# Kernel tuning notes

Measured on AMD Instinct MI355X. Metric: run time of the kernel, lower is better.

The kernel has to match this reference:

```python
import jax, jax.numpy as jnp
import numpy as np

C = 64          # channels (init arg)
G = 64          # input latent grid side -> output grid side 2G = 128
S = 2 * G + 2   # padded side for injective key encoding (coords shifted by +1)
N_IN = 60_000


def _encode(coords):
    # injective int32 key for 3D coords in [-1, 2G]
    c = coords + 1
    return (c[:, 0] * S + c[:, 1]) * S + c[:, 2]


def _lookup(keys_sorted, order, query_keys):
    # returns (row index into original arrays, found mask)
    n = keys_sorted.shape[0]
    pos = jnp.clip(jnp.searchsorted(keys_sorted, query_keys), 0, n - 1)
    found = keys_sorted[pos] == query_keys
    return order[pos], found


def _sparse_conv(out_coords, feats, W, b, keys_sorted, order, offsets):
    # Minkowski stride-1 conv: out[i] = sum_k feats[nbr(i, off_k)] @ W[k] + b
    acc = jnp.zeros((out_coords.shape[0], W.shape[-1]), feats.dtype)
    for k in range(offsets.shape[0]):  # 27 fixed kernel offsets
        idx, found = _lookup(keys_sorted, order, _encode(out_coords + offsets[k]))
        nb = jnp.where(found[:, None], feats[idx], jnp.zeros((), feats.dtype))
        acc = acc + nb @ W[k]
    return acc + b


def setup_inputs() -> dict:
    rng = np.random.default_rng(0)
    lin = rng.choice(G ** 3, size=N_IN, replace=False)  # unique occupied voxels
    coords = np.stack([lin // (G * G), (lin // G) % G, lin % G], axis=1).astype(np.int32)
    key = jax.random.key(0)
    ks = jax.random.split(key, 7)
    sc = 0.05
    return {
        'coords': jnp.asarray(coords),
        'feats': jax.random.normal(ks[0], (N_IN, C), jnp.float32),
        'W_up': jax.random.normal(ks[1], (8, C, C), jnp.float32) * sc,
        'b_up': jax.random.normal(ks[2], (C,), jnp.float32) * sc,
        'W1': jax.random.normal(ks[3], (27, C, C), jnp.float32) * sc,
        'b1': jax.random.normal(ks[4], (C,), jnp.float32) * sc,
        'W2': jax.random.normal(ks[5], (27, C, C), jnp.float32) * sc,
        'b2': jax.random.normal(ks[6], (C,), jnp.float32) * sc,
    }


def reference(coords, feats, W_up, b_up, W1, b1, W2, b2):
    # generative transpose conv (kernel 2, stride 2): 8 unique children per voxel
    child = jnp.array([[i, j, k] for i in (0, 1) for j in (0, 1) for k in (0, 1)], jnp.int32)
    out_coords = (2 * coords[:, None, :] + child[None]).reshape(-1, 3)  # [8N, 3]
    x = jnp.einsum('nc,kcd->nkd', feats, W_up).reshape(-1, C) + b_up     # [8N, C]
    x = jax.nn.relu(x)
    # shared kernel-map structure for both stride-1 convs
    keys = _encode(out_coords)
    order = jnp.argsort(keys)
    keys_sorted = keys[order]
    offs = jnp.array([[i, j, k] for i in (-1, 0, 1) for j in (-1, 0, 1) for k in (-1, 0, 1)], jnp.int32)
    x = jax.nn.relu(_sparse_conv(out_coords, x, W1, b1, keys_sorted, order, offs))
    x = _sparse_conv(out_coords, x, W2, b2, keys_sorted, order, offs)
    return x
```

## Files before the change

### kernel.cpp

```cpp
#include <hip/hip_runtime.h>
#include <stdint.h>

typedef __bf16 bf16x8 __attribute__((ext_vector_type(8)));
typedef float f32x4 __attribute__((ext_vector_type(4)));
typedef unsigned short ushort_t;

#define NPARENT 60000
#define NOUT (NPARENT*8)
#define ZIDX NOUT
#define TBL_N (66*66*66)
#define NBIN 4096

static constexpr size_t OFF_TABLE = 0;
static constexpr size_t OFF_CS    = 1152000;
static constexpr size_t OFF_Y     = OFF_CS + 960000;
static constexpr size_t OFF_HIST  = OFF_Y;
static constexpr size_t OFF_CNT   = OFF_Y + 16384;
static constexpr size_t OFF_Z     = OFF_Y + (size_t)(NOUT+1)*128;
static constexpr size_t OFF_FEATB = OFF_Z + (size_t)(NOUT+1)*128;
static constexpr size_t OFF_WUPF  = OFF_FEATB + (size_t)NPARENT*128;
static constexpr size_t OFF_W1F   = OFF_WUPF + (size_t)8*8192;
static constexpr size_t OFF_W2F   = OFF_W1F + (size_t)27*8192;
static constexpr size_t WS_NEED   = OFF_W2F + (size_t)27*8192;

__device__ __forceinline__ ushort_t f2bf(float x) {
  uint32_t u = __float_as_uint(x);
  u += 0x7fffu + ((u >> 16) & 1u);
  return (ushort_t)(u >> 16);
}

__device__ __forceinline__ int binof(int x, int y, int z) {
  int bx = x >> 2, by = y >> 2, bz = z >> 2, m = 0;
  #pragma unroll
  for (int b = 0; b < 4; ++b)
    m |= (((bx>>b)&1) << (3*b+2)) | (((by>>b)&1) << (3*b+1)) | (((bz>>b)&1) << (3*b));
  return m;
}

__device__ __forceinline__ void gl2lds16(const void* g, void* l) {
  __builtin_amdgcn_global_load_lds(
      (const __attribute__((address_space(1))) uint32_t*)g,
      (__attribute__((address_space(3))) uint32_t*)l, 16, 0, 0);
}

__global__ void k_zero(ushort_t* y, ushort_t* z) {
  int t = threadIdx.x;
  if (t < 64) y[(size_t)ZIDX*64 + t] = 0;
  else        z[(size_t)ZIDX*64 + (t-64)] = 0;
}

__global__ void k_hist(const int* __restrict__ coords, int* __restrict__ hist) {
  int i = blockIdx.x*blockDim.x + threadIdx.x;
  if (i >= NPARENT) return;
  atomicAdd(&hist[binof(coords[3*i], coords[3*i+1], coords[3*i+2])], 1);
}

__global__ void k_scan(const int* __restrict__ hist, int* __restrict__ cnt) {
  __shared__ int s[256];
  int t = threadIdx.x;
  int loc[16], sum = 0;
  #pragma unroll
  for (int j=0;j<16;++j){ loc[j]=hist[t*16+j]; sum+=loc[j]; }
  s[t]=sum;
  __syncthreads();
  if (t==0){ int a=0; for (int i=0;i<256;++i){ int v=s[i]; s[i]=a; a+=v; } }
  __syncthreads();
  int a=s[t];
  #pragma unroll
  for (int j=0;j<16;++j){ cnt[t*16+j]=a; a+=loc[j]; }
}

__global__ void k_rank(const int* __restrict__ coords, int* __restrict__ cnt,
                       int4* __restrict__ cs, int* __restrict__ tbl) {
  int i = blockIdx.x*blockDim.x + threadIdx.x;
  if (i >= NPARENT) return;
  int x = coords[3*i], y = coords[3*i+1], z = coords[3*i+2];
  int r = atomicAdd(&cnt[binof(x,y,z)], 1);
  cs[r] = make_int4(x, y, z, i);
  tbl[((x+1)*66 + (y+1))*66 + (z+1)] = r;
}

__global__ void k_feats_bf16(const float4* __restrict__ f, const int4* __restrict__ cs,
                             ushort_t* __restrict__ o, int total) {
  int t = blockIdx.x*blockDim.x + threadIdx.x;
  if (t >= total) return;
  int p = t >> 4, q = t & 15;
  int i = cs[p].w;
  float4 v = f[(size_t)i*16 + q];
  size_t ob = (size_t)p*64 + q*4;
  o[ob+0] = f2bf(v.x); o[ob+1] = f2bf(v.y);
  o[ob+2] = f2bf(v.z); o[ob+3] = f2bf(v.w);
}

__global__ void k_wfrag(const float* __restrict__ w, ushort_t* __restrict__ o, int total) {
  int i = blockIdx.x*blockDim.x + threadIdx.x;
  if (i >= total) return;
  int k = i >> 12, r = i & 4095, c = r >> 6, d = r & 63;
  int nt = d >> 4, lp = d & 15, ks = c >> 5, hi = (c >> 3) & 3, e = c & 7;
  int fi = ks*4 + nt, lane = hi*16 + lp;
  o[(size_t)(k*8 + fi)*512 + lane*8 + e] = f2bf(w[i]);
}

__global__ __launch_bounds__(256) void k_up(const ushort_t* __restrict__ featb,
    const ushort_t* __restrict__ wupf, const float* __restrict__ bup,
    ushort_t* __restrict__ y)
{
  int wave = threadIdx.x >> 6, lane = threadIdx.x & 63;
  int n0 = blockIdx.x*64 + wave*16;
  if (n0 >= NPARENT) return;
  int lp = lane & 15, hi = lane >> 4;
  const ushort_t* ar = featb + (size_t)(n0+lp)*64 + hi*8;
  bf16x8 a0 = *(const bf16x8*)(ar);
  bf16x8 a1 = *(const bf16x8*)(ar + 32);
  float bv[4];
  #pragma unroll
  for (int nt=0; nt<4; ++nt) bv[nt] = bup[nt*16+lp];
  for (int c8=0; c8<8; ++c8) {
    const ushort_t* wb = wupf + (size_t)c8*4096 + lane*8;
    f32x4 acc[4];
    #pragma unroll
    for (int nt=0;nt<4;++nt) acc[nt] = (f32x4){0.f,0.f,0.f,0.f};
    #pragma unroll
    for (int nt=0;nt<4;++nt)
      acc[nt] = __builtin_amdgcn_mfma_f32_16x16x32_bf16(a0, *(const bf16x8*)(wb + nt*512), acc[nt], 0,0,0);
    #pragma unroll
    for (int nt=0;nt<4;++nt)
      acc[nt] = __builtin_amdgcn_mfma_f32_16x16x32_bf16(a1, *(const bf16x8*)(wb + (4+nt)*512), acc[nt], 0,0,0);
    #pragma unroll
    for (int nt=0;nt<4;++nt) {
      #pragma unroll
      for (int j=0;j<4;++j) {
        int par = n0 + hi*4 + j;
        float v = acc[nt][j] + bv[nt];
        v = fmaxf(v, 0.f);
        y[(size_t)(par*8 + c8)*64 + nt*16 + lp] = f2bf(v);
      }
    }
  }
}

template<int RELU, int SCATTER, typename OUT_T>
__global__ __launch_bounds__(256) void k_conv(const int4* __restrict__ cs,
    const int* __restrict__ tbl, const ushort_t* __restrict__ fin,
    const ushort_t* __restrict__ wf, const float* __restrict__ bias,
    OUT_T* __restrict__ out)
{
  __shared__ __align__(16) int nbrs[32*27];
  __shared__ __align__(16) ushort_t bbuf[2][4096];

  int bid = blockIdx.x;
  int xcd = bid & 7, jj = bid >> 3;
  int wg = (xcd < 3 ? xcd*235 : 705 + (xcd-3)*234) + jj;

  int tid = threadIdx.x;
  int wave = tid >> 6, lane = tid & 63;
  int m0 = wg*256 + wave*64;
  int lp = lane & 15, hi = lane >> 4;
  int pblk0 = wg*32;

  for (int i = tid; i < 32*27; i += 256) {
    int p = i / 27, j = i - p*27;
    int4 cc = cs[pblk0 + p];
    int dx = j/9 - 1, dy = (j/3)%3 - 1, dz = j%3 - 1;
    nbrs[i] = tbl[((cc.x+dx+1)*66 + (cc.y+dy+1))*66 + (cc.z+dz+1)];
  }

  {
    const char* wb = (const char*)wf;
    #pragma unroll
    for (int j=0;j<2;++j) {
      int chunk = wave*2 + j;
      gl2lds16(wb + (size_t)chunk*1024 + lane*16, &bbuf[0][chunk*512]);
    }
  }

  int cx = (lp>>2)&1, cy = (lp>>1)&1, cz = lp&1, c = lp&7;
  int plbase = wave*8 + (lp>>3);

  f32x4 acc[4][4];
  #pragma unroll
  for (int s=0;s<4;++s)
    #pragma unroll
    for (int nt=0;nt<4;++nt) acc[s][nt] = (f32x4){0.f,0.f,0.f,0.f};

  const char* finl = (const char*)fin + hi*16;

  __syncthreads();

  uint32_t aoffc[4];
  {
    int idx = ((cx-1)>>1)*9 + ((cy-1)>>1)*3 + ((cz-1)>>1) + 13;
    int cpx = c ^ 7;
    #pragma unroll
    for (int s=0;s<4;++s) {
      int rank = nbrs[(plbase + s*2)*27 + idx];
      uint32_t off = (uint32_t)(rank*8 + cpx) * 128u;
      aoffc[s] = (rank < 0) ? (uint32_t)ZIDX*128u : off;
    }
  }

  #pragma unroll 1
  for (int k=0;k<27;++k) {
    int cur = k & 1;
    bf16x8 a[4][2];
    #pragma unroll
    for (int s=0;s<4;++s) {
      a[s][0] = *(const bf16x8*)(finl + aoffc[s]);
      a[s][1] = *(const bf16x8*)(finl + aoffc[s] + 64);
    }
    if (k < 26) {
      const char* wb = (const char*)wf + (size_t)(k+1)*8192;
      #pragma unroll
      for (int j=0;j<2;++j) {
        int chunk = wave*2 + j;
        gl2lds16(wb + (size_t)chunk*1024 + lane*16, &bbuf[cur^1][chunk*512]);
      }
    }
    bf16x8 bfr[8];
    #pragma unroll
    for (int f=0;f<8;++f) bfr[f] = *(const bf16x8*)&bbuf[cur][f*512 + lane*8];
    uint32_t aoffn[4];
    if (k < 26) {
      int k2 = k+1;
      int ox = k2/9 - 1, oy = (k2/3)%3 - 1, oz = k2%3 - 1;
      int xk = ((ox&1)<<2) | ((oy&1)<<1) | (oz&1);
      int cpx = c ^ xk;
      int idx = ((cx+ox)>>1)*9 + ((cy+oy)>>1)*3 + ((cz+oz)>>1) + 13;
      #pragma unroll
      for (int s=0;s<4;++s) {
        int rank = nbrs[(plbase + s*2)*27 + idx];
        uint32_t off = (uint32_t)(rank*8 + cpx) * 128u;
        aoffn[s] = (rank < 0) ? (uint32_t)ZIDX*128u : off;
      }
    }
    #pragma unroll
    for (int s=0;s<4;++s)
      #pragma unroll
      for (int nt=0;nt<4;++nt)
        acc[s][nt] = __builtin_amdgcn_mfma_f32_16x16x32_bf16(a[s][0], bfr[nt], acc[s][nt], 0,0,0);
    #pragma unroll
    for (int s=0;s<4;++s)
      #pragma unroll
      for (int nt=0;nt<4;++nt)
        acc[s][nt] = __builtin_amdgcn_mfma_f32_16x16x32_bf16(a[s][1], bfr[4+nt], acc[s][nt], 0,0,0);

    #pragma unroll
    for (int s=0;s<4;++s) aoffc[s] = aoffn[s];

    __syncthreads();
  }

  float bv[4];
  #pragma unroll
  for (int nt=0;nt<4;++nt) bv[nt] = bias[nt*16+lp];
  #pragma unroll
  for (int s=0;s<4;++s) {
    #pragma unroll
    for (int j=0;j<4;++j) {
      int row = m0 + s*16 + hi*4 + j;
      size_t rb;
      if constexpr (SCATTER) {
        int4 cc = cs[row >> 3];
        rb = ((size_t)cc.w*8 + (row & 7)) * 64;
      } else {
        rb = (size_t)row * 64;
      }
      #pragma unroll
      for (int nt=0;nt<4;++nt) {
        float v = acc[s][nt][j] + bv[nt];
        if (RELU) v = fmaxf(v, 0.f);
        size_t oi = rb + nt*16 + lp;
        if constexpr (sizeof(OUT_T)==2) ((ushort_t*)out)[oi] = f2bf(v);
        else                            out[oi] = v;
      }
    }
  }
}

extern "C" void kernel_launch(void* const* d_in, const int* in_sizes, int n_in,
                              void* d_out, int out_size, void* d_ws, size_t ws_size,
                              hipStream_t stream) {
  const int*   coords = (const int*)d_in[0];
  const float* feats  = (const float*)d_in[1];
  const float* Wup    = (const float*)d_in[2];
  const float* bup    = (const float*)d_in[3];
  const float* W1     = (const float*)d_in[4];
  const float* b1     = (const float*)d_in[5];
  const float* W2     = (const float*)d_in[6];
  const float* b2     = (const float*)d_in[7];
  char* ws = (char*)d_ws;
  if (ws_size < WS_NEED) return;

  int*      tbl  = (int*)(ws + OFF_TABLE);
  int4*     cs   = (int4*)(ws + OFF_CS);
  int*      hist = (int*)(ws + OFF_HIST);
  int*      cnt  = (int*)(ws + OFF_CNT);
  ushort_t* y    = (ushort_t*)(ws + OFF_Y);
  ushort_t* z    = (ushort_t*)(ws + OFF_Z);
  ushort_t* fb   = (ushort_t*)(ws + OFF_FEATB);
  ushort_t* wupf = (ushort_t*)(ws + OFF_WUPF);
  ushort_t* w1f  = (ushort_t*)(ws + OFF_W1F);
  ushort_t* w2f  = (ushort_t*)(ws + OFF_W2F);

  hipMemsetAsync(tbl, 0xFF, (size_t)TBL_N*4, stream);
  hipMemsetAsync(hist, 0, (size_t)NBIN*4, stream);
  k_zero<<<1,128,0,stream>>>(y, z);
  k_hist<<<(NPARENT+255)/256,256,0,stream>>>(coords, hist);
  k_scan<<<1,256,0,stream>>>(hist, cnt);
  k_rank<<<(NPARENT+255)/256,256,0,stream>>>(coords, cnt, cs, tbl);
  k_feats_bf16<<<(NPARENT*16+255)/256,256,0,stream>>>((const float4*)feats, cs, fb, NPARENT*16);
  k_wfrag<<<(8*4096+255)/256,256,0,stream>>>(Wup, wupf, 8*4096);
  k_wfrag<<<(27*4096+255)/256,256,0,stream>>>(W1, w1f, 27*4096);
  k_wfrag<<<(27*4096+255)/256,256,0,stream>>>(W2, w2f, 27*4096);
  k_up<<<(NPARENT+63)/64,256,0,stream>>>(fb, wupf, bup, y);
  k_conv<1,0,ushort_t><<<NOUT/256,256,0,stream>>>(cs, tbl, y,  w1f, b1, z);
  k_conv<0,1,float>   <<<NOUT/256,256,0,stream>>>(cs, tbl, z,  w2f, b2, (float*)d_out);
}
```

Before: 377.5 us.

## Stage block-local input rows in swizzled LDS to serve intra-block neighbor gathers

The conv kernel now preloads the block's own 32 parents' 256 feature rows into a new 32KB XOR-swizzled shared buffer. Neighbor lookups whose rank falls inside the block read from LDS; other lookups still gather from global memory, and in-block lanes point their global load at the zero row. The aim is to cut global/L2 gather traffic, since many 3x3x3 neighbors are siblings in the same parent block. In exchange, LDS use per block grows a lot, which may reduce occupancy, and both loads are issued every iteration with a per-lane select between them.

```diff
diff --git a/kernel.cpp b/kernel.cpp
--- a/kernel.cpp
+++ b/kernel.cpp
@@ -8,6 +8,7 @@
 #define NPARENT 60000
 #define NOUT (NPARENT*8)
 #define ZIDX NOUT
+#define ZOFF ((uint32_t)ZIDX*128u)
 #define TBL_N (66*66*66)
 #define NBIN 4096
 
@@ -147,6 +148,7 @@
 {
   __shared__ __align__(16) int nbrs[32*27];
   __shared__ __align__(16) ushort_t bbuf[2][4096];
+  __shared__ __align__(16) ushort_t abuf[256*64];
 
   int bid = blockIdx.x;
   int xcd = bid & 7, jj = bid >> 3;
@@ -166,6 +168,17 @@
   }
 
   {
+    const char* ybase = (const char*)fin + (size_t)pblk0*1024;
+    #pragma unroll
+    for (int j=0;j<8;++j) {
+      int rowloc = wave*64 + j*8 + (lane>>3);
+      int c = lane & 7;
+      gl2lds16(ybase + rowloc*128 + ((c ^ (rowloc&7))<<4),
+               (char*)abuf + wave*8192 + j*1024);
+    }
+  }
+
+  {
     const char* wb = (const char*)wf;
     #pragma unroll
     for (int j=0;j<2;++j) {
@@ -184,29 +197,36 @@
     for (int nt=0;nt<4;++nt) acc[s][nt] = (f32x4){0.f,0.f,0.f,0.f};
 
   const char* finl = (const char*)fin + hi*16;
+  const char* abufc = (const char*)abuf;
 
   __syncthreads();
 
-  uint32_t aoffc[4];
+  uint32_t agc[4]; uint32_t alc[4]; bool ibc[4];
+  uint32_t x0c, x1c;
   {
+    int xk = 7, cpx = c ^ xk;
     int idx = ((cx-1)>>1)*9 + ((cy-1)>>1)*3 + ((cz-1)>>1) + 13;
-    int cpx = c ^ 7;
+    x0c = (uint32_t)((hi ^ cpx) << 4);
+    x1c = (uint32_t)(((hi+4) ^ cpx) << 4);
     #pragma unroll
     for (int s=0;s<4;++s) {
       int rank = nbrs[(plbase + s*2)*27 + idx];
-      uint32_t off = (uint32_t)(rank*8 + cpx) * 128u;
-      aoffc[s] = (rank < 0) ? (uint32_t)ZIDX*128u : off;
+      int rloc = rank - pblk0;
+      bool ib = (unsigned)rloc < 32u;
+      ibc[s] = ib;
+      alc[s] = ib ? (uint32_t)((rloc*8 + cpx) << 7) : 0u;
+      agc[s] = (ib || rank < 0) ? ZOFF : (uint32_t)(rank*8 + cpx) * 128u;
     }
   }
 
   #pragma unroll 1
   for (int k=0;k<27;++k) {
     int cur = k & 1;
-    bf16x8 a[4][2];
+    bf16x8 g[4][2];
     #pragma unroll
     for (int s=0;s<4;++s) {
-      a[s][0] = *(const bf16x8*)(finl + aoffc[s]);
-      a[s][1] = *(const bf16x8*)(finl + aoffc[s] + 64);
+      g[s][0] = *(const bf16x8*)(finl + agc[s]);
+      g[s][1] = *(const bf16x8*)(finl + agc[s] + 64);
     }
     if (k < 26) {
       const char* wb = (const char*)wf + (size_t)(k+1)*8192;
@@ -219,19 +239,40 @@
     bf16x8 bfr[8];
     #pragma unroll
     for (int f=0;f<8;++f) bfr[f] = *(const bf16x8*)&bbuf[cur][f*512 + lane*8];
-    uint32_t aoffn[4];
+    bf16x8 l[4][2];
+    #pragma unroll
+    for (int s=0;s<4;++s) {
+      l[s][0] = *(const bf16x8*)(abufc + alc[s] + x0c);
+      l[s][1] = *(const bf16x8*)(abufc + alc[s] + x1c);
+    }
+    uint32_t agn[4]; uint32_t aln[4]; bool ibn[4];
+    uint32_t x0n = x0c, x1n = x1c;
     if (k < 26) {
       int k2 = k+1;
       int ox = k2/9 - 1, oy = (k2/3)%3 - 1, oz = k2%3 - 1;
       int xk = ((ox&1)<<2) | ((oy&1)<<1) | (oz&1);
       int cpx = c ^ xk;
       int idx = ((cx+ox)>>1)*9 + ((cy+oy)>>1)*3 + ((cz+oz)>>1) + 13;
+      x0n = (uint32_t)((hi ^ cpx) << 4);
+      x1n = (uint32_t)(((hi+4) ^ cpx) << 4);
       #pragma unroll
       for (int s=0;s<4;++s) {
         int rank = nbrs[(plbase + s*2)*27 + idx];
-        uint32_t off = (uint32_t)(rank*8 + cpx) * 128u;
-        aoffn[s] = (rank < 0) ? (uint32_t)ZIDX*128u : off;
-      }
+        int rloc = rank - pblk0;
+        bool ib = (unsigned)rloc < 32u;
+        ibn[s] = ib;
+        aln[s] = ib ? (uint32_t)((rloc*8 + cpx) << 7) : 0u;
+        agn[s] = (ib || rank < 0) ? ZOFF : (uint32_t)(rank*8 + cpx) * 128u;
+      }
+    } else {
+      #pragma unroll
+      for (int s=0;s<4;++s) { agn[s]=agc[s]; aln[s]=alc[s]; ibn[s]=ibc[s]; }
+    }
+    bf16x8 a[4][2];
+    #pragma unroll
+    for (int s=0;s<4;++s) {
+      a[s][0] = ibc[s] ? l[s][0] : g[s][0];
+      a[s][1] = ibc[s] ? l[s][1] : g[s][1];
     }
     #pragma unroll
     for (int s=0;s<4;++s)
@@ -245,7 +286,8 @@
         acc[s][nt] = __builtin_amdgcn_mfma_f32_16x16x32_bf16(a[s][1], bfr[4+nt], acc[s][nt], 0,0,0);
 
     #pragma unroll
-    for (int s=0;s<4;++s) aoffc[s] = aoffn[s];
+    for (int s=0;s<4;++s) { agc[s]=agn[s]; alc[s]=aln[s]; ibc[s]=ibn[s]; }
+    x0c = x0n; x1c = x1n;
 
     __syncthreads();
   }
```

Result: faster. 308.0 us (-18.4%).
